# Kernel tuning notes

Hardware: AMD Instinct MI355X
Metric: run time of the kernel (lower is better)

## Reference

```python
import jax, jax.numpy as jnp
import numpy as np

B, DIM, RANK, H, W = 16, 64, 32, 128, 128
E, K, BINS, FREQ_DIM, KS = 4, 2, 8, 64, 7
NOISE_STD = 1.0 / E


def dwconv(x, w, b, pad):
    # depthwise conv, NCHW, weight [C,1,kh,kw]
    y = jax.lax.conv_general_dilated(x, w, (1, 1), [(pad, pad), (pad, pad)],
        dimension_numbers=('NCHW', 'OIHW', 'NCHW'), feature_group_count=x.shape[1])
    return y + b[None, :, None, None]


def avgpool3(x):
    # AvgPool2d(3, stride=1, padding=1), count_include_pad=True -> sum/9
    s = jax.lax.reduce_window(x, 0.0, jax.lax.add, (1, 1, 3, 3), (1, 1, 1, 1),
        [(0, 0), (0, 0), (1, 1), (1, 1)])
    return s / 9.0


def freq_filter(x, gain, decay, cmax):
    # HighFreqGlobal / LowFreqGlobal: rfft2 -> scale magnitude by radial filter -> irfft2
    Bh, C, Hh, Wh = x.shape
    xf = jnp.fft.rfft2(x, norm='ortho')
    mag, ph = jnp.abs(xf), jnp.angle(xf)
    fy = jnp.fft.fftfreq(Hh).astype(x.dtype)[:, None]
    fx = jnp.fft.rfftfreq(Wh).astype(x.dtype)[None, :]
    fg = jnp.sqrt(fy ** 2 + fx ** 2)
    filt = jnp.clip((1.0 - jnp.exp(-gain * fg)) * jnp.exp(-decay * fg), 0.0, cmax)
    return jnp.fft.irfft2((mag * filt) * jnp.exp(1j * ph), s=(Hh, Wh), norm='ortho')


def freq_energy(x):
    # RoutingFunction.get_frequency_energy: radial energy histogram over BINS bins
    Bh, C, Hh, Wh = x.shape
    mag = jnp.abs(jnp.fft.fft2(x, norm='forward'))
    gy = jnp.arange(-Hh // 2, Hh // 2, dtype=jnp.float32)[:, None]
    gx = jnp.arange(-Wh // 2, Wh // 2, dtype=jnp.float32)[None, :]
    dist = jnp.sqrt(gy ** 2 + gx ** 2)
    edges = jnp.linspace(0.0, dist.max(), BINS + 1)
    masks = ((dist[None] >= edges[:-1, None, None]) & (dist[None] < edges[1:, None, None])).astype(mag.dtype)
    return jnp.einsum('bchw,khw->bk', mag, masks) / C  # sum over HW then mean over C


def setup_inputs():
    key = jax.random.key(0)
    ks = jax.random.split(key, 16)
    p = lambda k, shp, s=0.02: jax.random.normal(k, shp, jnp.float32) * s
    return {
        'x': jax.random.normal(ks[0], (B, DIM, H, W), jnp.float32),
        'noise': jax.random.normal(ks[1], (B, E), jnp.float32),
        'gate_w': p(ks[2], (E, DIM)),
        'fg_w1': p(ks[3], (FREQ_DIM, BINS)),
        'fg_b1': jnp.zeros((FREQ_DIM,), jnp.float32),
        'fg_w2': p(ks[4], (E, FREQ_DIM)),
        'proj0': p(ks[5], (E, RANK, DIM)),
        'proj1': p(ks[6], (E, RANK, DIM)),
        'proj2': p(ks[7], (E, DIM, RANK)),
        'hg_gain': jnp.float32(2.0),
        'hg_decay': jnp.float32(0.5),
        'hf_w1': p(ks[8], (RANK, 1, 3, 3), 0.1),
        'hf_b1': jnp.zeros((RANK,), jnp.float32),
        'hf_w2': p(ks[9], (RANK, 1, 3, 3), 0.1),
        'hf_b2': jnp.zeros((RANK,), jnp.float32),
        'lg_gain': jnp.float32(1.0),
        'lg_decay': jnp.float32(1.0),
        'lf_w': p(ks[10], (RANK, 1, KS, KS), 0.1),
        'lf_b': jnp.zeros((RANK,), jnp.float32),
    }


def reference(x, noise, gate_w, fg_w1, fg_b1, fg_w2, proj0, proj1, proj2,
              hg_gain, hg_decay, hf_w1, hf_b1, hf_w2, hf_b2,
              lg_gain, lg_decay, lf_w, lf_b):
    Bh = x.shape[0]
    # routing: image gate (GAP + linear) + frequency gate (MLP on radial energy)
    img_logits = jnp.mean(x, axis=(2, 3)) @ gate_w.T
    femb = freq_energy(x)
    hidden = jax.nn.relu(femb @ fg_w1.T + fg_b1)
    logits = img_logits + hidden @ fg_w2.T
    scores = jax.nn.softmax(logits + noise * NOISE_STD, axis=-1)
    vals, idx = jax.lax.top_k(scores, K)
    gates = jnp.zeros_like(scores).at[jnp.arange(Bh)[:, None], idx].set(vals)

    def expert(e, body):
        # ModExpert.process: low-rank proj -> body * silu(gate proj of shared=x) -> up proj + shortcut
        h = jnp.einsum('bchw,rc->brhw', x, proj0[e])
        g = jax.nn.silu(jnp.einsum('bchw,rc->brhw', x, proj1[e]))
        h = body(h) * g
        return jnp.einsum('brhw,cr->bchw', h, proj2[e]) + x

    gelu = lambda z: jax.nn.gelu(z, approximate=False)
    bodies = [
        lambda z: freq_filter(z, hg_gain, hg_decay, 3.0),                          # HighFreqGlobal
        lambda z: dwconv(gelu(dwconv(z, hf_w1, hf_b1, 1)), hf_w2, hf_b2, 1),       # HighFreqLocal
        lambda z: freq_filter(z, lg_gain, lg_decay, 1.0),                          # LowFreqGlobal
        lambda z: avgpool3(gelu(dwconv(z, lf_w, lf_b, KS // 2))),                  # LowFreqLocal
    ]
    # dispatch/combine expressed densely: gates are exactly zero for non-selected experts,
    # so weighted sum == SparseDispatcher.combine
    out = jnp.zeros_like(x)
    for e, body in enumerate(bodies):
        out = out + gates[:, e][:, None, None, None] * expert(e, body)
    return out
```

## Files before the change

kernel.cpp:

```cpp
#include <hip/hip_runtime.h>
#include <math.h>


namespace {

struct cpx { float x, y; };
struct TwB {
  cpx t0;
  cpx ws[6];
  float sg[6];
};

using bf16x8 = __attribute__((ext_vector_type(8))) short;
using f32x4  = __attribute__((ext_vector_type(4))) float;

__device__ __forceinline__ short f2bf(float f){
  unsigned u = __float_as_uint(f);
  u += 0x7FFF + ((u >> 16) & 1);
  return (short)(u >> 16);
}

__device__ __forceinline__ cpx cmul(cpx a, cpx b){ return {a.x*b.x - a.y*b.y, a.x*b.y + a.y*b.x}; }

__device__ __forceinline__ cpx tw(int k, float invN){
  float s, c;
  sincosf(-6.283185307179586f * (float)k * invN, &s, &c);
  return {c, s};
}

__device__ __forceinline__ void init_twb(TwB &T, int lane){
  T.t0 = tw(lane, 1.0f/128.0f);
  int m = 32;
  #pragma unroll
  for (int s = 0; s < 6; s++){
    bool up = (lane & m) != 0;
    cpx w = tw(lane & (m-1), 1.0f/(float)(2*m));
    T.ws[s] = up ? w : cpx{1.0f, 0.0f};
    T.sg[s] = up ? -1.0f : 1.0f;
    m >>= 1;
  }
}

__device__ __forceinline__ int br6(int l){ return (int)(__brev((unsigned)l) >> 26); }
__device__ __forceinline__ int pos7(int j){ return ((j & 1) << 6) | (j >> 1); }

__device__ __forceinline__ void fft128(cpx &a, cpx &b, int lane, const TwB &T){
  cpx u{a.x + b.x, a.y + b.y};
  cpx v{a.x - b.x, a.y - b.y};
  v = cmul(v, T.t0);
  a = u; b = v;
  int m = 32;
  #pragma unroll
  for (int s = 0; s < 6; s++){
    float pax = __shfl_xor(a.x, m);
    float pay = __shfl_xor(a.y, m);
    float pbx = __shfl_xor(b.x, m);
    float pby = __shfl_xor(b.y, m);
    float sg = T.sg[s];
    cpx w = T.ws[s];
    cpx ta{fmaf(sg, a.x, pax), fmaf(sg, a.y, pay)};
    cpx tb{fmaf(sg, b.x, pbx), fmaf(sg, b.y, pby)};
    a = cmul(ta, w);
    b = cmul(tb, w);
    m >>= 1;
  }
}

__device__ __forceinline__ float gelu_exact(float v){
  return 0.5f * v * (1.0f + erff(v * 0.70710678118654752f));
}

__device__ __forceinline__ float silu(float v){
  return v / (1.0f + expf(-v));
}


__global__ __launch_bounds__(512) void k_fft2fwd(const float* __restrict__ x, float2* __restrict__ X,
                                                 float* __restrict__ part_w, float* __restrict__ xmean){
  __shared__ float2 z[8192];
  int bc = blockIdx.x; int t = threadIdx.x;
  int lane = t & 63, wv = t >> 6;
  TwB T; init_twb(T, lane);
  const float* img = x + (size_t)bc * 16384;
  int rb = br6(lane);

  #pragma unroll 4
  for (int k = 0; k < 8; k++){
    int p = wv*8 + k;
    int h0 = 2*p, h1 = 2*p + 1;
    cpx a{img[h0*128 + lane],      img[h1*128 + lane]};
    cpx b{img[h0*128 + lane + 64], img[h1*128 + lane + 64]};
    fft128(a, b, lane, T);
    int ia = (p << 7) | (rb ^ p);
    z[ia]      = make_float2(a.x, a.y);
    z[ia | 64] = make_float2(b.x, b.y);
  }
  __syncthreads();

  float rax[8], ray[8], rbx[8], rby[8];
  #pragma unroll
  for (int k = 0; k < 8; k++){
    int jj = wv*8 + k;
    int p  = lane >> 1, s = lane & 1;
    int p2 = 32 + p;
    cpx a, b;
    if (jj == 0){
      float2 z0  = z[(p << 7)  | (0  ^ p)];
      float2 z64 = z[(p << 7)  | (32 ^ p)];
      float2 w0  = z[(p2 << 7) | (0  ^ p2)];
      float2 w64 = z[(p2 << 7) | (32 ^ p2)];
      a = { s ? z0.y : z0.x, s ? z64.y : z64.x };
      b = { s ? w0.y : w0.x, s ? w64.y : w64.x };
    } else {
      int jm = 128 - jj;
      int pj = pos7(jj), pm = pos7(jm);
      float2 z1 = z[(p << 7) | (pj ^ p)],  z2 = z[(p << 7) | (pm ^ p)];
      if (s == 0) a = { 0.5f*(z1.x + z2.x), 0.5f*(z1.y - z2.y) };
      else        a = { 0.5f*(z1.y + z2.y), 0.5f*(z2.x - z1.x) };
      float2 w1 = z[(p2 << 7) | (pj ^ p2)], w2 = z[(p2 << 7) | (pm ^ p2)];
      if (s == 0) b = { 0.5f*(w1.x + w2.x), 0.5f*(w1.y - w2.y) };
      else        b = { 0.5f*(w1.y + w2.y), 0.5f*(w2.x - w1.x) };
    }
    fft128(a, b, lane, T);
    rax[k] = a.x; ray[k] = a.y; rbx[k] = b.x; rby[k] = b.y;
  }
  __syncthreads();
  #pragma unroll
  for (int k = 0; k < 8; k++){
    int jj = wv*8 + k;
    int ia = (jj << 7) | (rb ^ jj);
    z[ia]      = make_float2(rax[k], ray[k]);
    z[ia | 64] = make_float2(rbx[k], rby[k]);
  }
  __syncthreads();

  if (t == 0) xmean[bc] = z[0].x * (1.0f/16384.0f);

  float edges[9];
  float step = sqrtf(8192.0f) * 0.125f;
  #pragma unroll
  for (int k = 0; k <= 8; k++) edges[k] = step * (float)k;
  float acc[8] = {0,0,0,0,0,0,0,0};
  for (int idx = t; idx < 64*128; idx += 512){
    int j = idx >> 7, i = idx & 127;
    if (j == 0){
      float2 c0 = z[pos7(i)];
      int in_ = (128 - i) & 127;
      float2 d0v = z[pos7(in_)];
      float x0r = 0.5f*(c0.x + d0v.x), x0i = 0.5f*(c0.y - d0v.y);
      float x6r = 0.5f*(c0.y + d0v.y), x6i = 0.5f*(d0v.x - c0.x);
      float m0 = sqrtf(x0r*x0r + x0i*x0i) * (1.0f/16384.0f);
      float m6 = sqrtf(x6r*x6r + x6i*x6i) * (1.0f/16384.0f);
      float dyv = (float)(i - 64);
      float d0 = sqrtf(dyv*dyv + 4096.0f);
      float d6 = fabsf(dyv);
      #pragma unroll
      for (int k = 0; k < 8; k++){
        if (d0 >= edges[k] && d0 < edges[k+1]) acc[k] += m0;
        if (d6 >= edges[k] && d6 < edges[k+1]) acc[k] += m6;
      }
    } else {
      float2 zv = z[(j << 7) | (pos7(i) ^ j)];
      float mag = sqrtf(zv.x*zv.x + zv.y*zv.y) * (2.0f/16384.0f);
      float dy = (float)(i - 64), dx = (float)(j - 64);
      float d = sqrtf(dy*dy + dx*dx);
      #pragma unroll
      for (int k = 0; k < 8; k++)
        if (d >= edges[k] && d < edges[k+1]) acc[k] += mag;
    }
  }
  #pragma unroll
  for (int k = 0; k < 8; k++){
    float v = acc[k];
    for (int off = 32; off > 0; off >>= 1) v += __shfl_xor(v, off);
    if (lane == 0) part_w[(bc*8 + wv)*8 + k] = v;
  }

  float2* Xo = X + (size_t)bc * (65*128);
  for (int idx = t; idx < 65*128; idx += 512){
    int j = idx >> 7, i = idx & 127;
    float2 v;
    if (j == 0){
      float2 c0 = z[pos7(i)];
      int in_ = (128 - i) & 127;
      float2 d0v = z[pos7(in_)];
      v = make_float2(0.5f*(c0.x + d0v.x), 0.5f*(c0.y - d0v.y));
    } else if (j == 64){
      float2 c0 = z[pos7(i)];
      int in_ = (128 - i) & 127;
      float2 d0v = z[pos7(in_)];
      v = make_float2(0.5f*(c0.y + d0v.y), 0.5f*(d0v.x - c0.x));
    } else {
      v = z[(j << 7) | (pos7(i) ^ j)];
    }
    Xo[idx] = v;
  }
}

__global__ __launch_bounds__(128) void k_routing(const float* __restrict__ xmean, const float* __restrict__ part_w,
    const float* __restrict__ noise, const float* __restrict__ gate_w,
    const float* __restrict__ fg_w1, const float* __restrict__ fg_b1, const float* __restrict__ fg_w2,
    int* __restrict__ slot_e, int* __restrict__ slot_of, float* __restrict__ slot_g){
  __shared__ float femb[16][8];
  __shared__ float hid[16][64];
  __shared__ float lgt[16][4];
  int t = threadIdx.x;
  {
    int b = t >> 3, k = t & 7;
    float s = 0.f;
    for (int c = 0; c < 64; c++)
      for (int w = 0; w < 8; w++)
        s += part_w[((b*64 + c)*8 + w)*8 + k];
    femb[b][k] = s * (1.0f/64.0f);
  }
  __syncthreads();
  for (int idx = t; idx < 16*64; idx += 128){
    int b = idx >> 6, f = idx & 63;
    float s = fg_b1[f];
    for (int k = 0; k < 8; k++) s += femb[b][k] * fg_w1[f*8 + k];
    hid[b][f] = fmaxf(s, 0.f);
  }
  __syncthreads();
  if (t < 64){
    int b = t >> 2, e = t & 3;
    float s = 0.f;
    for (int c = 0; c < 64; c++) s += xmean[b*64 + c] * gate_w[e*64 + c];
    for (int f = 0; f < 64; f++) s += hid[b][f] * fg_w2[e*64 + f];
    lgt[b][e] = s + noise[b*4 + e] * 0.25f;
  }
  __syncthreads();
  if (t < 16){
    int b = t;
    float m = fmaxf(fmaxf(lgt[b][0], lgt[b][1]), fmaxf(lgt[b][2], lgt[b][3]));
    float p[4]; float sum = 0.f;
    for (int e = 0; e < 4; e++){ p[e] = expf(lgt[b][e] - m); sum += p[e]; }
    for (int e = 0; e < 4; e++) p[e] /= sum;
    int i1 = 0;
    for (int e = 1; e < 4; e++) if (p[e] > p[i1]) i1 = e;
    int i2 = -1;
    for (int e = 0; e < 4; e++){ if (e == i1) continue; if (i2 < 0 || p[e] > p[i2]) i2 = e; }
    slot_e[b*2 + 0] = i1;
    slot_e[b*2 + 1] = i2;
    slot_g[b*2 + 0] = p[i1];
    slot_g[b*2 + 1] = p[i2];
    for (int e = 0; e < 4; e++) slot_of[b*4 + e] = (e == i1) ? 0 : ((e == i2) ? 1 : -1);
  }
}

__global__ __launch_bounds__(256) void k_transW(const float* __restrict__ proj0, float* __restrict__ p0t){
  int t = threadIdx.x;
  for (int idx = t; idx < 2048; idx += 256){
    int r = idx >> 6, c = idx & 63;
    p0t[0*2048 + c*32 + r] = proj0[0*2048 + idx];
    p0t[1*2048 + c*32 + r] = proj0[2*2048 + idx];
  }
}

__global__ __launch_bounds__(256) void k_projfreq(const float2* __restrict__ X, const float* __restrict__ p0t,
    float2* __restrict__ Y, const int* __restrict__ slot_e,
    const float* __restrict__ hg_gain, const float* __restrict__ hg_decay,
    const float* __restrict__ lg_gain, const float* __restrict__ lg_decay){
  int b = blockIdx.z;
  int e0 = __builtin_amdgcn_readfirstlane(slot_e[b*2 + 0]);
  int e1 = __builtin_amdgcn_readfirstlane(slot_e[b*2 + 1]);
  bool f0 = (e0 == 0) || (e0 == 2);
  bool f1 = (e1 == 0) || (e1 == 2);
  if (!f0 && !f1) return;
  int j = blockIdx.y;
  int i0 = blockIdx.x * 64;
  int t = threadIdx.x;
  int lane = t & 63;
  int w = __builtin_amdgcn_readfirstlane(t >> 6);
  __shared__ float2 sx[64][64];
  for (int idx = t; idx < 4096; idx += 256){
    int c = idx >> 6, ii = idx & 63;
    sx[c][ii] = X[(((size_t)(b*64 + c))*65 + j)*128 + i0 + ii];
  }
  __syncthreads();
  int i = i0 + lane;
  const float* W0 = p0t + ((f0 ? (e0 >> 1) : (e1 >> 1)) * 2048) + w*8;
  const float* W1 = p0t + ((f1 ? (e1 >> 1) : (e0 >> 1)) * 2048) + w*8;
  float a0x[8] = {0,0,0,0,0,0,0,0}, a0y[8] = {0,0,0,0,0,0,0,0};
  float a1x[8] = {0,0,0,0,0,0,0,0}, a1y[8] = {0,0,0,0,0,0,0,0};
  for (int c = 0; c < 64; c++){
    float2 xv = sx[c][lane];
    const float* wc0 = W0 + c*32;
    const float* wc1 = W1 + c*32;
    #pragma unroll
    for (int k = 0; k < 8; k++){
      float w0v = wc0[k];
      a0x[k] += w0v * xv.x; a0y[k] += w0v * xv.y;
      float w1v = wc1[k];
      a1x[k] += w1v * xv.x; a1y[k] += w1v * xv.y;
    }
  }
  float fy = (float)(i < 64 ? i : i - 128) * (1.0f/128.0f);
  float fx = (float)j * (1.0f/128.0f);
  float fg = sqrtf(fy*fy + fx*fx);
  if (f0){
    float gain, decay, cmax;
    if (e0 == 0){ gain = *hg_gain; decay = *hg_decay; cmax = 3.0f; }
    else        { gain = *lg_gain; decay = *lg_decay; cmax = 1.0f; }
    float filt = (1.0f - expf(-gain*fg)) * expf(-decay*fg);
    filt = fminf(fmaxf(filt, 0.0f), cmax) * (1.0f/16384.0f);
    int bs = b*2 + 0;
    #pragma unroll
    for (int k = 0; k < 8; k++){
      int r = w*8 + k;
      Y[((size_t)(bs*32 + r))*8320 + j*128 + i] = make_float2(a0x[k]*filt, a0y[k]*filt);
    }
  }
  if (f1){
    float gain, decay, cmax;
    if (e1 == 0){ gain = *hg_gain; decay = *hg_decay; cmax = 3.0f; }
    else        { gain = *lg_gain; decay = *lg_decay; cmax = 1.0f; }
    float filt = (1.0f - expf(-gain*fg)) * expf(-decay*fg);
    filt = fminf(fmaxf(filt, 0.0f), cmax) * (1.0f/16384.0f);
    int bs = b*2 + 1;
    #pragma unroll
    for (int k = 0; k < 8; k++){
      int r = w*8 + k;
      Y[((size_t)(bs*32 + r))*8320 + j*128 + i] = make_float2(a1x[k]*filt, a1y[k]*filt);
    }
  }
}

__global__ __launch_bounds__(512) void k_ifft2(float2* __restrict__ Y, const int* __restrict__ slot_e){
  int blk = blockIdx.x;
  int bs = blk >> 5, r = blk & 31;
  int es = slot_e[bs];
  if (es == 1 || es == 3) return;
  __shared__ float2 z[8192];
  int t = threadIdx.x; int lane = t & 63, wv = t >> 6;
  TwB T; init_twb(T, lane);
  int rb = br6(lane);
  float2* Yb = Y + (size_t)(bs*32 + r) * 8320;

  for (int idx = t; idx < 8192; idx += 512){
    int j = idx >> 7, i = idx & 127;
    if (j == 0){
      float2 y0 = Yb[i];
      float2 y6 = Yb[8192 + i];
      z[pos7(i)] = make_float2(y0.x - y6.y, y0.y + y6.x);
    } else {
      z[(j << 7) | (pos7(i) ^ j)] = Yb[idx];
    }
  }
  __syncthreads();

  #pragma unroll
  for (int k = 0; k < 8; k++){
    int jj = wv*8 + k;
    float2 z0 = z[(jj << 7) | (pos7(lane) ^ jj)];
    float2 z1 = z[(jj << 7) | ((pos7(lane) + 32) ^ jj)];
    cpx a{z0.x, -z0.y}, b{z1.x, -z1.y};
    fft128(a, b, lane, T);
    int ia = (jj << 7) | (rb ^ jj);
    z[ia]      = make_float2(a.x, -a.y);
    z[ia | 64] = make_float2(b.x, -b.y);
  }
  __syncthreads();

  float* body = (float*)Yb;
  #pragma unroll 2
  for (int k = 0; k < 8; k++){
    int p = wv*8 + k;
    int h = 2*p, h1 = 2*p + 1;
    int ph = pos7(h), ph1 = pos7(h1);
    cpx a, b;
    if (lane == 0){
      float2 c0 = z[ph], c1 = z[ph1];
      a = { c0.x, c1.x };
      b = { c0.y, c1.y };
    } else {
      float2 yh = z[(lane << 7) | (ph ^ lane)];
      float2 y1 = z[(lane << 7) | (ph1 ^ lane)];
      a = { yh.x - y1.y, yh.y + y1.x };
      int lm = 64 - lane;
      float2 zh  = z[(lm << 7) | (ph ^ lm)];
      float2 z1_ = z[(lm << 7) | (ph1 ^ lm)];
      b = { zh.x + z1_.y, z1_.x - zh.y };
    }
    a.y = -a.y; b.y = -b.y;
    fft128(a, b, lane, T);
    int n0 = 2*rb;
    body[h*128 + n0]      = a.x;
    body[h1*128 + n0]     = -a.y;
    body[h*128 + n0 + 1]  = b.x;
    body[h1*128 + n0 + 1] = -b.y;
  }
}

__global__ __launch_bounds__(256) void k_projA(const float* __restrict__ x, const float* __restrict__ proj0,
    const int* __restrict__ slot_e, float* __restrict__ A){
  int b = blockIdx.y;
  int e0 = slot_e[b*2 + 0], e1 = slot_e[b*2 + 1];
  bool c0 = (e0 == 1) || (e0 == 3);
  bool c1 = (e1 == 1) || (e1 == 3);
  if (!c0 && !c1) return;
  int hw = blockIdx.x * 256 + threadIdx.x;
  const float* xb = x + (size_t)b*64*16384 + hw;
  float xv[64];
  #pragma unroll
  for (int c = 0; c < 64; c++) xv[c] = xb[(size_t)c*16384];
  if (c0){
    const float* W = proj0 + __builtin_amdgcn_readfirstlane(e0)*2048;
    float* Ab = A + (size_t)(b*2 + 0)*32*16384 + hw;
    #pragma unroll 4
    for (int r = 0; r < 32; r++){
      float a = 0.f;
      #pragma unroll
      for (int c = 0; c < 64; c++) a += W[r*64 + c] * xv[c];
      Ab[(size_t)r*16384] = a;
    }
  }
  if (c1){
    const float* W = proj0 + __builtin_amdgcn_readfirstlane(e1)*2048;
    float* Ab = A + (size_t)(b*2 + 1)*32*16384 + hw;
    #pragma unroll 4
    for (int r = 0; r < 32; r++){
      float a = 0.f;
      #pragma unroll
      for (int c = 0; c < 64; c++) a += W[r*64 + c] * xv[c];
      Ab[(size_t)r*16384] = a;
    }
  }
}

__global__ __launch_bounds__(256) void k_conv3(const float* __restrict__ A, float* __restrict__ bodyY,
    const float* __restrict__ w1g, const float* __restrict__ b1g,
    const float* __restrict__ w2g, const float* __restrict__ b2g,
    const int* __restrict__ slot_of){
  int by = blockIdx.y; int b = by >> 5, r = by & 31;
  int slot = slot_of[b*4 + 1];
  if (slot < 0) return;
  int bs = b*2 + slot;
  int h0 = blockIdx.x * 16;
  int t = threadIdx.x;
  __shared__ float sin_[20*130];
  __shared__ float st[18*130];
  for (int i = t; i < 20*130; i += 256) sin_[i] = 0.f;
  for (int i = t; i < 18*130; i += 256) st[i] = 0.f;
  float w1[9], w2[9];
  #pragma unroll
  for (int k = 0; k < 9; k++){ w1[k] = w1g[r*9 + k]; w2[k] = w2g[r*9 + k]; }
  float b1 = b1g[r], b2 = b2g[r];
  __syncthreads();
  const float* ip = A + (size_t)(bs*32 + r)*16384;
  for (int idx = t; idx < 20*128; idx += 256){
    int li = idx >> 7, ww = idx & 127;
    int ih = h0 - 2 + li;
    if (ih >= 0 && ih < 128) sin_[li*130 + 1 + ww] = ip[ih*128 + ww];
  }
  __syncthreads();
  for (int idx = t; idx < 18*128; idx += 256){
    int li = idx >> 7, ww = idx & 127;
    int hs = h0 - 1 + li;
    if (hs >= 0 && hs < 128){
      float acc = b1;
      #pragma unroll
      for (int kh = 0; kh < 3; kh++)
        #pragma unroll
        for (int kw = 0; kw < 3; kw++)
          acc += w1[kh*3 + kw] * sin_[(li + kh)*130 + ww + kw];
      st[li*130 + 1 + ww] = gelu_exact(acc);
    }
  }
  __syncthreads();
  float* op = bodyY + (size_t)(bs*32 + r)*16640;
  for (int idx = t; idx < 16*128; idx += 256){
    int li = idx >> 7, ww = idx & 127;
    int ho = h0 + li;
    float acc = b2;
    #pragma unroll
    for (int kh = 0; kh < 3; kh++)
      #pragma unroll
      for (int kw = 0; kw < 3; kw++)
        acc += w2[kh*3 + kw] * st[(li + kh)*130 + ww + kw];
    op[ho*128 + ww] = acc;
  }
}

__global__ __launch_bounds__(256) void k_conv7(const float* __restrict__ A, float* __restrict__ bodyY,
    const float* __restrict__ wg, const float* __restrict__ bg,
    const int* __restrict__ slot_of){
  int by = blockIdx.y; int b = by >> 5, r = by & 31;
  int slot = slot_of[b*4 + 3];
  if (slot < 0) return;
  int bs = b*2 + slot;
  int h0 = blockIdx.x * 16;
  int t = threadIdx.x;
  __shared__ float sin_[24*134];
  __shared__ float st[18*134];
  __shared__ float wsh[49];
  for (int i = t; i < 24*134; i += 256) sin_[i] = 0.f;
  for (int i = t; i < 18*134; i += 256) st[i] = 0.f;
  if (t < 49) wsh[t] = wg[r*49 + t];
  float bias = bg[r];
  __syncthreads();
  const float* ip = A + (size_t)(bs*32 + r)*16384;
  for (int idx = t; idx < 24*128; idx += 256){
    int li = idx >> 7, ww = idx & 127;
    int ih = h0 - 4 + li;
    if (ih >= 0 && ih < 128) sin_[li*134 + 3 + ww] = ip[ih*128 + ww];
  }
  __syncthreads();
  for (int idx = t; idx < 18*128; idx += 256){
    int li = idx >> 7, ww = idx & 127;
    int hs = h0 - 1 + li;
    if (hs >= 0 && hs < 128){
      float acc = bias;
      #pragma unroll
      for (int kh = 0; kh < 7; kh++)
        #pragma unroll
        for (int kw = 0; kw < 7; kw++)
          acc += wsh[kh*7 + kw] * sin_[(li + kh)*134 + ww + kw];
      st[li*134 + 1 + ww] = gelu_exact(acc);
    }
  }
  __syncthreads();
  float* op = bodyY + (size_t)(bs*32 + r)*16640;
  for (int idx = t; idx < 16*128; idx += 256){
    int li = idx >> 7, ww = idx & 127;
    int ho = h0 + li;
    float acc = 0.f;
    #pragma unroll
    for (int kh = 0; kh < 3; kh++)
      #pragma unroll
      for (int kw = 0; kw < 3; kw++)
        acc += st[(li + kh)*134 + ww + kw];
    op[ho*128 + ww] = acc * (1.0f/9.0f);
  }
}

__global__ __launch_bounds__(256) void k_combine(const float* __restrict__ x, const float* __restrict__ bodyY,
    const float* __restrict__ proj1, const float* __restrict__ proj2,
    const int* __restrict__ slot_e, const float* __restrict__ slot_g,
    float* __restrict__ out){
  __shared__ unsigned short xs[128][72];
  __shared__ unsigned short bs2[2][128][36];
  __shared__ unsigned short sblk[4][2][16][40];
  int b = blockIdx.y;
  int px0 = blockIdx.x * 128;
  int t = threadIdx.x;
  int w = t >> 6, lane = t & 63;
  int h = lane & 15, g = lane >> 4;
  int ea = __builtin_amdgcn_readfirstlane(slot_e[b*2 + 0]);
  int eb = __builtin_amdgcn_readfirstlane(slot_e[b*2 + 1]);
  float ga = slot_g[b*2 + 0], gb = slot_g[b*2 + 1];
  float gs = ga + gb;

  const float* xb = x + (size_t)b*64*16384;
  float* ob = out + (size_t)b*64*16384;
  const float* Bd0 = bodyY + (size_t)(b*2 + 0)*32*16640;
  const float* Bd1 = bodyY + (size_t)(b*2 + 1)*32*16640;

  for (int idx = t; idx < 2048; idx += 256){
    int c = idx >> 5, pq = idx & 31;
    float4 v = *(const float4*)&xb[(size_t)c*16384 + px0 + pq*4];
    xs[pq*4 + 0][c] = (unsigned short)f2bf(v.x);
    xs[pq*4 + 1][c] = (unsigned short)f2bf(v.y);
    xs[pq*4 + 2][c] = (unsigned short)f2bf(v.z);
    xs[pq*4 + 3][c] = (unsigned short)f2bf(v.w);
  }
  for (int idx = t; idx < 2048; idx += 256){
    int s = idx >> 10, r = (idx >> 5) & 31, pq = idx & 31;
    const float* Bod = (s == 0) ? Bd0 : Bd1;
    float4 v = *(const float4*)&Bod[(size_t)r*16640 + px0 + pq*4];
    bs2[s][pq*4 + 0][r] = (unsigned short)f2bf(v.x);
    bs2[s][pq*4 + 1][r] = (unsigned short)f2bf(v.y);
    bs2[s][pq*4 + 2][r] = (unsigned short)f2bf(v.z);
    bs2[s][pq*4 + 3][r] = (unsigned short)f2bf(v.w);
  }

  bf16x8 a1[2][2][2];
  #pragma unroll
  for (int s = 0; s < 2; s++){
    const float* P1 = proj1 + (s == 0 ? ea : eb)*2048;
    #pragma unroll
    for (int mr = 0; mr < 2; mr++)
      #pragma unroll
      for (int k0 = 0; k0 < 2; k0++){
        const float* p = P1 + (mr*16 + h)*64 + k0*32 + g*8;
        bf16x8 v;
        #pragma unroll
        for (int j = 0; j < 8; j++) v[j] = f2bf(p[j]);
        a1[s][mr][k0] = v;
      }
  }
  bf16x8 a2[2][4];
  #pragma unroll
  for (int s = 0; s < 2; s++){
    const float* P2 = proj2 + (s == 0 ? ea : eb)*2048;
    #pragma unroll
    for (int mc = 0; mc < 4; mc++){
      const float* p = P2 + (mc*16 + h)*32 + g*8;
      bf16x8 v;
      #pragma unroll
      for (int j = 0; j < 8; j++) v[j] = f2bf(p[j]);
      a2[s][mc] = v;
    }
  }
  __syncthreads();

  int pxw = w*32;
  #pragma unroll
  for (int nt = 0; nt < 2; nt++){
    int pxl = pxw + nt*16;
    int px  = px0 + pxl;
    bf16x8 bx[2];
    #pragma unroll
    for (int k0 = 0; k0 < 2; k0++)
      bx[k0] = *(bf16x8*)&xs[pxl + h][k0*32 + g*8];
    f32x4 acc1[2][2];
    #pragma unroll
    for (int s = 0; s < 2; s++)
      #pragma unroll
      for (int mr = 0; mr < 2; mr++){
        f32x4 acc = {0.f, 0.f, 0.f, 0.f};
        acc = __builtin_amdgcn_mfma_f32_16x16x32_bf16(a1[s][mr][0], bx[0], acc, 0, 0, 0);
        acc = __builtin_amdgcn_mfma_f32_16x16x32_bf16(a1[s][mr][1], bx[1], acc, 0, 0, 0);
        acc1[s][mr] = acc;
      }
    #pragma unroll
    for (int s = 0; s < 2; s++){
      float gw = (s == 0) ? ga : gb;
      #pragma unroll
      for (int mr = 0; mr < 2; mr++){
        int r0 = mr*16 + g*4;
        unsigned short b4[4];
        *(uint2*)b4 = *(uint2*)&bs2[s][pxl + h][r0];
        unsigned pk0, pk1;
        {
          float bv0 = __uint_as_float(((unsigned)b4[0]) << 16);
          float bv1 = __uint_as_float(((unsigned)b4[1]) << 16);
          float bv2 = __uint_as_float(((unsigned)b4[2]) << 16);
          float bv3 = __uint_as_float(((unsigned)b4[3]) << 16);
          float s0 = gw * bv0 * silu(acc1[s][mr][0]);
          float s1 = gw * bv1 * silu(acc1[s][mr][1]);
          float s2 = gw * bv2 * silu(acc1[s][mr][2]);
          float s3 = gw * bv3 * silu(acc1[s][mr][3]);
          pk0 = (unsigned)(unsigned short)f2bf(s0) | ((unsigned)(unsigned short)f2bf(s1) << 16);
          pk1 = (unsigned)(unsigned short)f2bf(s2) | ((unsigned)(unsigned short)f2bf(s3) << 16);
        }
        uint2 pv; pv.x = pk0; pv.y = pk1;
        *(uint2*)&sblk[w][s][h][r0] = pv;
      }
    }
    bf16x8 sb0 = *(bf16x8*)&sblk[w][0][h][g*8];
    bf16x8 sb1 = *(bf16x8*)&sblk[w][1][h][g*8];
    f32x4 acc2[4];
    #pragma unroll
    for (int mc = 0; mc < 4; mc++){
      f32x4 acc = {0.f, 0.f, 0.f, 0.f};
      acc = __builtin_amdgcn_mfma_f32_16x16x32_bf16(a2[0][mc], sb0, acc, 0, 0, 0);
      acc = __builtin_amdgcn_mfma_f32_16x16x32_bf16(a2[1][mc], sb1, acc, 0, 0, 0);
      acc2[mc] = acc;
    }
    #pragma unroll
    for (int mc = 0; mc < 4; mc++)
      #pragma unroll
      for (int reg = 0; reg < 4; reg++){
        int c = mc*16 + g*4 + reg;
        size_t o = (size_t)c*16384 + px + h;
        ob[o] = gs * xb[o] + acc2[mc][reg];
      }
  }
}

}

extern "C" void kernel_launch(void* const* d_in, const int* in_sizes, int n_in,
                              void* d_out, int out_size, void* d_ws, size_t ws_size,
                              hipStream_t stream) {
  (void)in_sizes; (void)n_in; (void)out_size; (void)ws_size;
  const float* x        = (const float*)d_in[0];
  const float* noise    = (const float*)d_in[1];
  const float* gate_w   = (const float*)d_in[2];
  const float* fg_w1    = (const float*)d_in[3];
  const float* fg_b1    = (const float*)d_in[4];
  const float* fg_w2    = (const float*)d_in[5];
  const float* proj0    = (const float*)d_in[6];
  const float* proj1    = (const float*)d_in[7];
  const float* proj2    = (const float*)d_in[8];
  const float* hg_gain  = (const float*)d_in[9];
  const float* hg_decay = (const float*)d_in[10];
  const float* hf_w1    = (const float*)d_in[11];
  const float* hf_b1    = (const float*)d_in[12];
  const float* hf_w2    = (const float*)d_in[13];
  const float* hf_b2    = (const float*)d_in[14];
  const float* lg_gain  = (const float*)d_in[15];
  const float* lg_decay = (const float*)d_in[16];
  const float* lf_w     = (const float*)d_in[17];
  const float* lf_b     = (const float*)d_in[18];
  float* out = (float*)d_out;

  float* ws = (float*)d_ws;
  float2* X  = (float2*)ws;
  float*  A  = ws;
  float*  Yf = ws + 17039360;
  float2* Y2 = (float2*)Yf;
  float*  tail   = ws + 34078720;
  float*  xmean  = tail;
  float*  part_w = xmean + 1024;
  float*  p0t    = part_w + 65536;
  float*  slot_g = p0t + 4096;
  int*    slot_e = (int*)(slot_g + 32);
  int*    slot_of = slot_e + 32;

  k_transW<<<1, 256, 0, stream>>>(proj0, p0t);
  k_fft2fwd<<<1024, 512, 0, stream>>>(x, X, part_w, xmean);
  k_routing<<<1, 128, 0, stream>>>(xmean, part_w, noise, gate_w, fg_w1, fg_b1, fg_w2,
                                   slot_e, slot_of, slot_g);

  k_projfreq<<<dim3(2,65,16), 256, 0, stream>>>(X, p0t, Y2, slot_e,
                                                hg_gain, hg_decay, lg_gain, lg_decay);

  k_projA<<<dim3(64,16), 256, 0, stream>>>(x, proj0, slot_e, A);

  k_ifft2<<<1024, 512, 0, stream>>>(Y2, slot_e);

  k_conv3<<<dim3(8,512), 256, 0, stream>>>(A, Yf, hf_w1, hf_b1, hf_w2, hf_b2, slot_of);
  k_conv7<<<dim3(8,512), 256, 0, stream>>>(A, Yf, lf_w, lf_b, slot_of);

  k_combine<<<dim3(128,16), 256, 0, stream>>>(x, Yf, proj1, proj2, slot_e, slot_g, out);
}
```

Before: 354.8 us.

## Compute low-rank projection in k_projA with bf16 MFMA via shared-memory tile

Replaces the scalar per-pixel 64x32 FMA projection in k_projA with bf16 MFMA 16x16x32 instructions. The block now stages a 128-pixel by 64-channel bf16 tile of x in shared memory, converts the proj0 weights to bf16 fragments, and doubles the grid to cover 128 pixels per block. The aim is to move the projection arithmetic from vector ALUs onto matrix cores. In exchange, inputs and weights are rounded to bf16, which lowers accuracy, and the stores to A are now scattered 16-wide across rows rather than fully coalesced.

```diff
diff --git a/kernel.cpp b/kernel.cpp
--- a/kernel.cpp
+++ b/kernel.cpp
@@ -394,35 +394,72 @@
 __global__ __launch_bounds__(256) void k_projA(const float* __restrict__ x, const float* __restrict__ proj0,
     const int* __restrict__ slot_e, float* __restrict__ A){
   int b = blockIdx.y;
-  int e0 = slot_e[b*2 + 0], e1 = slot_e[b*2 + 1];
+  int e0 = __builtin_amdgcn_readfirstlane(slot_e[b*2 + 0]);
+  int e1 = __builtin_amdgcn_readfirstlane(slot_e[b*2 + 1]);
   bool c0 = (e0 == 1) || (e0 == 3);
   bool c1 = (e1 == 1) || (e1 == 3);
   if (!c0 && !c1) return;
-  int hw = blockIdx.x * 256 + threadIdx.x;
-  const float* xb = x + (size_t)b*64*16384 + hw;
-  float xv[64];
-  #pragma unroll
-  for (int c = 0; c < 64; c++) xv[c] = xb[(size_t)c*16384];
-  if (c0){
-    const float* W = proj0 + __builtin_amdgcn_readfirstlane(e0)*2048;
-    float* Ab = A + (size_t)(b*2 + 0)*32*16384 + hw;
-    #pragma unroll 4
-    for (int r = 0; r < 32; r++){
-      float a = 0.f;
-      #pragma unroll
-      for (int c = 0; c < 64; c++) a += W[r*64 + c] * xv[c];
-      Ab[(size_t)r*16384] = a;
-    }
-  }
-  if (c1){
-    const float* W = proj0 + __builtin_amdgcn_readfirstlane(e1)*2048;
-    float* Ab = A + (size_t)(b*2 + 1)*32*16384 + hw;
-    #pragma unroll 4
-    for (int r = 0; r < 32; r++){
-      float a = 0.f;
-      #pragma unroll
-      for (int c = 0; c < 64; c++) a += W[r*64 + c] * xv[c];
-      Ab[(size_t)r*16384] = a;
+  __shared__ unsigned short xs[128][72];
+  int px0 = blockIdx.x * 128;
+  int t = threadIdx.x;
+  int w = t >> 6, lane = t & 63;
+  int h = lane & 15, g = lane >> 4;
+  const float* xb = x + (size_t)b*64*16384;
+
+  for (int idx = t; idx < 2048; idx += 256){
+    int c = idx >> 5, pq = idx & 31;
+    float4 v = *(const float4*)&xb[(size_t)c*16384 + px0 + pq*4];
+    xs[pq*4 + 0][c] = (unsigned short)f2bf(v.x);
+    xs[pq*4 + 1][c] = (unsigned short)f2bf(v.y);
+    xs[pq*4 + 2][c] = (unsigned short)f2bf(v.z);
+    xs[pq*4 + 3][c] = (unsigned short)f2bf(v.w);
+  }
+
+  bf16x8 af[2][2][2];
+  #pragma unroll
+  for (int s = 0; s < 2; s++){
+    bool cv = (s == 0) ? c0 : c1;
+    if (!cv) continue;
+    int e = (s == 0) ? e0 : e1;
+    const float* P0 = proj0 + e*2048;
+    #pragma unroll
+    for (int mr = 0; mr < 2; mr++)
+      #pragma unroll
+      for (int k0 = 0; k0 < 2; k0++){
+        const float* p = P0 + (mr*16 + h)*64 + k0*32 + g*8;
+        bf16x8 v;
+        #pragma unroll
+        for (int j = 0; j < 8; j++) v[j] = f2bf(p[j]);
+        af[s][mr][k0] = v;
+      }
+  }
+  __syncthreads();
+
+  int pxw = w*32;
+  #pragma unroll
+  for (int nt = 0; nt < 2; nt++){
+    int pxl = pxw + nt*16;
+    int px  = px0 + pxl;
+    bf16x8 bx[2];
+    #pragma unroll
+    for (int k0 = 0; k0 < 2; k0++)
+      bx[k0] = *(bf16x8*)&xs[pxl + h][k0*32 + g*8];
+    #pragma unroll
+    for (int s = 0; s < 2; s++){
+      bool cv = (s == 0) ? c0 : c1;
+      if (!cv) continue;
+      float* Ab = A + (size_t)((b*2 + s)*32)*16384;
+      #pragma unroll
+      for (int mr = 0; mr < 2; mr++){
+        f32x4 acc = {0.f, 0.f, 0.f, 0.f};
+        acc = __builtin_amdgcn_mfma_f32_16x16x32_bf16(af[s][mr][0], bx[0], acc, 0, 0, 0);
+        acc = __builtin_amdgcn_mfma_f32_16x16x32_bf16(af[s][mr][1], bx[1], acc, 0, 0, 0);
+        #pragma unroll
+        for (int reg = 0; reg < 4; reg++){
+          int r = mr*16 + g*4 + reg;
+          Ab[(size_t)r*16384 + px + h] = acc[reg];
+        }
+      }
     }
   }
 }
@@ -716,7 +753,7 @@
   k_projfreq<<<dim3(2,65,16), 256, 0, stream>>>(X, p0t, Y2, slot_e,
                                                 hg_gain, hg_decay, lg_gain, lg_decay);
 
-  k_projA<<<dim3(64,16), 256, 0, stream>>>(x, proj0, slot_e, A);
+  k_projA<<<dim3(128,16), 256, 0, stream>>>(x, proj0, slot_e, A);
 
   k_ifft2<<<1024, 512, 0, stream>>>(Y2, slot_e);
 
```

Result: faster. 304.6 us (-14.1%).
